# Kernel optimization log

Measured on AMD Instinct MI355X. Metric: run time of the kernel, lower is better.

The kernel has to match this reference:

```python
import jax, jax.numpy as jnp
import numpy as np

N = 10000      # nodes
E = 160000     # edges
F_IN = 128     # input_feature
G = 64         # graphs in batch
NC = 10        # num_classes
H1, H2, H3 = 1000, 700, 200


def _xavier(k, fi, fo):
    lim = float(np.sqrt(6.0 / (fi + fo)))
    return jax.random.uniform(k, (fi, fo), jnp.float32, -lim, lim)


def setup_inputs() -> dict:
    key = jax.random.key(0)
    ks = jax.random.split(key, 8)
    x = jax.random.normal(ks[0], (N, F_IN), jnp.float32)
    edge_index = jax.random.randint(ks[1], (2, E), 0, N)
    batch = jnp.sort(jax.random.randint(ks[2], (N,), 0, G))
    return {
        "x": x,
        "edge_index": edge_index,
        "batch": batch,
        "W1": _xavier(ks[3], F_IN, H1), "b1": jnp.zeros((H1,), jnp.float32),
        "W2": _xavier(ks[4], H1, H2),   "b2": jnp.zeros((H2,), jnp.float32),
        "W3": _xavier(ks[5], H2, H3),   "b3": jnp.zeros((H3,), jnp.float32),
        "Wl": _xavier(ks[6], H3, NC),   "bl": jnp.zeros((NC,), jnp.float32),
    }


def _gcn_conv(x, W, b, src, dst, dinv):
    # GCNConv: h = xW; out_i = sum_{j->i} d_j^-1/2 d_i^-1/2 h_j + d_i^-1 h_i + b
    h = x @ W
    coef = dinv[src] * dinv[dst]                      # [E]
    agg = jax.ops.segment_sum(h[src] * coef[:, None], dst, num_segments=N)
    agg = agg + h * (dinv * dinv)[:, None]            # self-loop term
    return agg + b


def reference(x, edge_index, batch, W1, b1, W2, b2, W3, b3, Wl, bl):
    src, dst = edge_index[0], edge_index[1]
    # degree with self-loops (edge weight 1), computed on target nodes
    deg = jax.ops.segment_sum(jnp.ones((E,), x.dtype), dst, num_segments=N) + 1.0
    dinv = jax.lax.rsqrt(deg)

    h = jax.nn.relu(_gcn_conv(x, W1, b1, src, dst, dinv))
    h = jax.nn.relu(_gcn_conv(h, W2, b2, src, dst, dinv))
    h = jax.nn.relu(_gcn_conv(h, W3, b3, src, dst, dinv))

    # global_mean_pool over graph ids
    s = jax.ops.segment_sum(h, batch, num_segments=G)
    cnt = jax.ops.segment_sum(jnp.ones((N,), h.dtype), batch, num_segments=G)
    pooled = s / jnp.maximum(cnt, 1.0)[:, None]

    # dropout is identity in eval mode
    return pooled @ Wl + bl
```

## Files before the change

kernel.cpp:

```cpp
#include <hip/hip_runtime.h>
#include <hip/hip_bf16.h>
#include <stdint.h>


#define SLOT 64

__device__ __forceinline__ uint16_t f2b(float f) {
    union { float f; uint32_t u; } v; v.f = f;
    return (uint16_t)((v.u + 0x7fffu + ((v.u >> 16) & 1u)) >> 16);
}
__device__ __forceinline__ float blo(uint32_t u) { union { uint32_t u; float f; } v; v.u = u << 16; return v.f; }
__device__ __forceinline__ float bhi(uint32_t u) { union { uint32_t u; float f; } v; v.u = u & 0xffff0000u; return v.f; }

__global__ void k_scatter(const int* __restrict__ src, const int* __restrict__ dst,
                          int* __restrict__ cursor, int* __restrict__ slots, int E) {
    int e = blockIdx.x * blockDim.x + threadIdx.x;
    if (e < E) {
        int s = src[e], d = dst[e];
        int pos = atomicAdd(&cursor[d], 1);
        if (pos < SLOT) slots[d * SLOT + pos] = s;
    }
}

__global__ void k_prep(const float* __restrict__ W1, const float* __restrict__ W2,
                       const float* __restrict__ W3,
                       uint16_t* __restrict__ T1, uint16_t* __restrict__ T2,
                       uint16_t* __restrict__ T3,
                       const float* __restrict__ b1, const float* __restrict__ b2,
                       const float* __restrict__ b3,
                       float* __restrict__ p1, float* __restrict__ p2,
                       float* __restrict__ p3,
                       const float* __restrict__ x, uint16_t* __restrict__ xb,
                       const int* __restrict__ deg, float* __restrict__ dinv,
                       int N, int F, int H1, int H2, int H3,
                       int Fp, int H1p, int H2p, int H3p, int n8) {
    __shared__ float tile[32][33];
    int z = blockIdx.z;
    if (z < 3) {
        const float* W; uint16_t* T; int K, Nn, Kp, Np;
        if (z == 0)      { W = W1; T = T1; K = F;  Nn = H1; Kp = Fp;  Np = H1p; }
        else if (z == 1) { W = W2; T = T2; K = H1; Nn = H2; Kp = H1p; Np = H2p; }
        else             { W = W3; T = T3; K = H2; Nn = H3; Kp = H2p; Np = H3p; }
        if ((int)blockIdx.x * 32 >= Kp || (int)blockIdx.y * 32 >= Np) return;
        int k0 = blockIdx.x * 32, n0 = blockIdx.y * 32;
        int tx = threadIdx.x, ty = threadIdx.y;
        for (int i = ty; i < 32; i += 8) {
            int k = k0 + i, n = n0 + tx;
            tile[i][tx] = (k < K && n < Nn) ? W[(size_t)k * Nn + n] : 0.f;
        }
        __syncthreads();
        for (int i = ty; i < 32; i += 8) {
            int n = n0 + i, k = k0 + tx;
            T[(size_t)n * Kp + k] = f2b(tile[tx][i]);
        }
    } else {
        int id = (blockIdx.y * gridDim.x + blockIdx.x) * 256 + threadIdx.y * 32 + threadIdx.x;
        if (z == 3) {
            if (id < H1p) p1[id] = (id < H1) ? b1[id] : 0.f;
            else if (id < H1p + H2p) { int k = id - H1p; p2[k] = (k < H2) ? b2[k] : 0.f; }
            else if (id < H1p + H2p + H3p) { int k = id - H1p - H2p; p3[k] = (k < H3) ? b3[k] : 0.f; }
        } else if (z == 4) {
            if (id < n8) {
                const float4* x4 = (const float4*)x;
                float4 a = x4[2 * id], b = x4[2 * id + 1];
                uint4 o;
                o.x = (uint32_t)f2b(a.x) | ((uint32_t)f2b(a.y) << 16);
                o.y = (uint32_t)f2b(a.z) | ((uint32_t)f2b(a.w) << 16);
                o.z = (uint32_t)f2b(b.x) | ((uint32_t)f2b(b.y) << 16);
                o.w = (uint32_t)f2b(b.z) | ((uint32_t)f2b(b.w) << 16);
                ((uint4*)xb)[id] = o;
            }
        } else {
            if (id < N) dinv[id] = rsqrtf((float)deg[id] + 1.0f);
        }
    }
}

__global__ __launch_bounds__(256) void k_agg_panel(
    const uint16_t* __restrict__ in, uint16_t* __restrict__ out,
    const int* __restrict__ deg_, const int* __restrict__ slots,
    const float* __restrict__ dinv, const float* __restrict__ bias,
    int N, int Hc, int pc, int P, int relu) {
    int slotg = blockIdx.x & 7;
    int panel = slotg % P;
    int seg   = slotg / P;
    int nseg  = 8 / P;
    int segLen = (N + nseg - 1) / nseg;
    int wave = threadIdx.x >> 6, lane = threadIdx.x & 63;
    int half = lane >> 5, sub = lane & 31;
    int item = (blockIdx.x >> 3) * 128 + wave * 32 + sub;
    int rel = item / pc;
    if (rel >= segLen) return;
    int node = seg * segLen + rel;
    if (node >= N) return;
    int j = panel * pc + (item - rel * pc);
    int deg = deg_[node];
    if (deg > SLOT) deg = SLOT;
    int base = node * SLOT;
    float dv = dinv[node];
    const uint4* in4 = (const uint4*)in;
    float a[8] = {0.f, 0.f, 0.f, 0.f, 0.f, 0.f, 0.f, 0.f};
    if (half == 0) {
        float self = dv * dv;
        uint4 v = in4[(size_t)node * Hc + j];
        a[0] = self * blo(v.x); a[1] = self * bhi(v.x);
        a[2] = self * blo(v.y); a[3] = self * bhi(v.y);
        a[4] = self * blo(v.z); a[5] = self * bhi(v.z);
        a[6] = self * blo(v.w); a[7] = self * bhi(v.w);
    }
    int D8 = deg & ~7;
    for (int e = 4 * half; e < D8; e += 8) {
        int4 q = *(const int4*)&slots[base + e];
        uint4 h0 = in4[(size_t)q.x * Hc + j];
        uint4 h1 = in4[(size_t)q.y * Hc + j];
        uint4 h2 = in4[(size_t)q.z * Hc + j];
        uint4 h3 = in4[(size_t)q.w * Hc + j];
        float c0 = dinv[q.x] * dv, c1 = dinv[q.y] * dv;
        float c2 = dinv[q.z] * dv, c3 = dinv[q.w] * dv;
        a[0] += c0 * blo(h0.x); a[1] += c0 * bhi(h0.x);
        a[2] += c0 * blo(h0.y); a[3] += c0 * bhi(h0.y);
        a[4] += c0 * blo(h0.z); a[5] += c0 * bhi(h0.z);
        a[6] += c0 * blo(h0.w); a[7] += c0 * bhi(h0.w);
        a[0] += c1 * blo(h1.x); a[1] += c1 * bhi(h1.x);
        a[2] += c1 * blo(h1.y); a[3] += c1 * bhi(h1.y);
        a[4] += c1 * blo(h1.z); a[5] += c1 * bhi(h1.z);
        a[6] += c1 * blo(h1.w); a[7] += c1 * bhi(h1.w);
        a[0] += c2 * blo(h2.x); a[1] += c2 * bhi(h2.x);
        a[2] += c2 * blo(h2.y); a[3] += c2 * bhi(h2.y);
        a[4] += c2 * blo(h2.z); a[5] += c2 * bhi(h2.z);
        a[6] += c2 * blo(h2.w); a[7] += c2 * bhi(h2.w);
        a[0] += c3 * blo(h3.x); a[1] += c3 * bhi(h3.x);
        a[2] += c3 * blo(h3.y); a[3] += c3 * bhi(h3.y);
        a[4] += c3 * blo(h3.z); a[5] += c3 * bhi(h3.z);
        a[6] += c3 * blo(h3.w); a[7] += c3 * bhi(h3.w);
    }
    int t0 = half ? (D8 + 4 < deg ? D8 + 4 : deg) : D8;
    int t1 = half ? deg : (D8 + 4 < deg ? D8 + 4 : deg);
    for (int e = t0; e < t1; ++e) {
        int s0 = slots[base + e];
        uint4 h = in4[(size_t)s0 * Hc + j];
        float c = dinv[s0] * dv;
        a[0] += c * blo(h.x); a[1] += c * bhi(h.x);
        a[2] += c * blo(h.y); a[3] += c * bhi(h.y);
        a[4] += c * blo(h.z); a[5] += c * bhi(h.z);
        a[6] += c * blo(h.w); a[7] += c * bhi(h.w);
    }
#pragma unroll
    for (int t = 0; t < 8; ++t) a[t] += __shfl_xor(a[t], 32, 64);
    if (half == 0) {
        if (bias) {
            const float4* b4 = (const float4*)bias;
            float4 b0 = b4[2 * j], b1 = b4[2 * j + 1];
            a[0] += b0.x; a[1] += b0.y; a[2] += b0.z; a[3] += b0.w;
            a[4] += b1.x; a[5] += b1.y; a[6] += b1.z; a[7] += b1.w;
        }
        if (relu) {
#pragma unroll
            for (int t = 0; t < 8; ++t) a[t] = fmaxf(a[t], 0.f);
        }
        uint4 o;
        o.x = (uint32_t)f2b(a[0]) | ((uint32_t)f2b(a[1]) << 16);
        o.y = (uint32_t)f2b(a[2]) | ((uint32_t)f2b(a[3]) << 16);
        o.z = (uint32_t)f2b(a[4]) | ((uint32_t)f2b(a[5]) << 16);
        o.w = (uint32_t)f2b(a[6]) | ((uint32_t)f2b(a[7]) << 16);
        ((uint4*)out)[(size_t)node * Hc + j] = o;
    }
}

__global__ __launch_bounds__(256) void k_pool_fast(
    const uint16_t* __restrict__ h, const int* __restrict__ batch,
    float* __restrict__ pooled_sum, int N, int H, int Hp) {
    int j    = threadIdx.x & 63;
    int slot = threadIdx.x >> 6;
    int Hc   = H >> 2;
    if (j >= Hc) return;
    int HcP  = Hp >> 2;
    const uint2* h2 = (const uint2*)h;
    int base = (blockIdx.x * 4 + slot) * 16;
    float a0 = 0.f, a1 = 0.f, a2 = 0.f, a3 = 0.f;
    int gcur = -1;
#pragma unroll 4
    for (int t = 0; t < 16; ++t) {
        int node = base + t;
        if (node < N) {
            int g = batch[node];
            if (g != gcur) {
                if (gcur >= 0) {
                    float* ps = &pooled_sum[(size_t)gcur * H + j * 4];
                    atomicAdd(&ps[0], a0); atomicAdd(&ps[1], a1);
                    atomicAdd(&ps[2], a2); atomicAdd(&ps[3], a3);
                }
                gcur = g; a0 = a1 = a2 = a3 = 0.f;
            }
            uint2 v = h2[(size_t)node * HcP + j];
            a0 += blo(v.x); a1 += bhi(v.x);
            a2 += blo(v.y); a3 += bhi(v.y);
        }
    }
    if (gcur >= 0) {
        float* ps = &pooled_sum[(size_t)gcur * H + j * 4];
        atomicAdd(&ps[0], a0); atomicAdd(&ps[1], a1);
        atomicAdd(&ps[2], a2); atomicAdd(&ps[3], a3);
    }
}

typedef __attribute__((ext_vector_type(8))) short short8;
typedef __attribute__((ext_vector_type(4))) float floatx4;

#define LDSP(p) ((__attribute__((address_space(3))) void*)(uintptr_t)(p))
#define GLBP(p) ((const __attribute__((address_space(1))) void*)(uintptr_t)(p))

__global__ __launch_bounds__(256) void k_gemm128(
    const uint16_t* __restrict__ A, const uint16_t* __restrict__ Bt,
    const float* __restrict__ bias, uint16_t* __restrict__ Cout,
    int M, int Kp, int Np, int relu) {
    __shared__ uint16_t As[128 * 64];
    __shared__ uint16_t Bs[128 * 64];
    int tid = threadIdx.x;
    int wave = tid >> 6, lane = tid & 63;
    int quad = lane >> 4, m16 = lane & 15;
    int wr = wave >> 1, wc = wave & 1;
    int row0 = blockIdx.y * 128, col0 = blockIdx.x * 128;

    int rA = tid >> 3;
    int cA = (tid & 7) ^ (rA & 7);
    const uint16_t* gA = A  + (size_t)(row0 + rA) * Kp + cA * 8;
    const uint16_t* gB = Bt + (size_t)(col0 + rA) * Kp + cA * 8;
    uint16_t* lA = As + tid * 8;
    uint16_t* lB = Bs + tid * 8;
    size_t rowStep32 = (size_t)32 * Kp;

    floatx4 acc[4][4];
#pragma unroll
    for (int i = 0; i < 4; ++i)
#pragma unroll
        for (int j = 0; j < 4; ++j) acc[i][j] = (floatx4){0.f, 0.f, 0.f, 0.f};

    const short* Ash = (const short*)As;
    const short* Bsh = (const short*)Bs;
    int swA = m16 & 7;

    for (int k0 = 0; k0 < Kp; k0 += 64) {
#pragma unroll
        for (int p = 0; p < 4; ++p) {
            __builtin_amdgcn_global_load_lds(GLBP(gA + p * rowStep32), LDSP(lA + p * 2048), 16, 0, 0);
            __builtin_amdgcn_global_load_lds(GLBP(gB + p * rowStep32), LDSP(lB + p * 2048), 16, 0, 0);
        }
        gA += 64; gB += 64;
        __syncthreads();
#pragma unroll
        for (int h = 0; h < 2; ++h) {
            short8 af[4], bf[4];
            int c = h * 4 + quad;
            int pos = (c ^ swA) * 8;
#pragma unroll
            for (int i = 0; i < 4; ++i)
                af[i] = *(const short8*)&Ash[(wr * 64 + i * 16 + m16) * 64 + pos];
#pragma unroll
            for (int j = 0; j < 4; ++j)
                bf[j] = *(const short8*)&Bsh[(wc * 64 + j * 16 + m16) * 64 + pos];
#pragma unroll
            for (int i = 0; i < 4; ++i)
#pragma unroll
                for (int j = 0; j < 4; ++j)
                    acc[i][j] = __builtin_amdgcn_mfma_f32_16x16x32_bf16(af[i], bf[j], acc[i][j], 0, 0, 0);
        }
        __syncthreads();
    }

    float bv[4];
#pragma unroll
    for (int j = 0; j < 4; ++j) {
        int n = col0 + wc * 64 + j * 16 + m16;
        bv[j] = bias ? bias[n] : 0.f;
    }
#pragma unroll
    for (int i = 0; i < 4; ++i) {
        int mBase = row0 + wr * 64 + i * 16 + quad * 4;
#pragma unroll
        for (int r = 0; r < 4; ++r) {
            int m = mBase + r;
            if (m < M) {
#pragma unroll
                for (int j = 0; j < 4; ++j) {
                    int n = col0 + wc * 64 + j * 16 + m16;
                    float v = acc[i][j][r] + bv[j];
                    if (relu) v = fmaxf(v, 0.f);
                    Cout[(size_t)m * Np + n] = f2b(v);
                }
            }
        }
    }
}

__global__ __launch_bounds__(256) void k_gemm64(
    const uint16_t* __restrict__ A, const uint16_t* __restrict__ Bt,
    const float* __restrict__ bias, uint16_t* __restrict__ Cout,
    int M, int Kp, int Np, int relu) {
    __shared__ uint16_t As[128 * 64];
    __shared__ uint16_t Bs[64 * 64];
    int tid = threadIdx.x;
    int wave = tid >> 6, lane = tid & 63;
    int quad = lane >> 4, m16 = lane & 15;
    int wr = wave >> 1, wc = wave & 1;
    int row0 = blockIdx.y * 128, col0 = blockIdx.x * 64;

    int rA = tid >> 3;
    int cA = (tid & 7) ^ (rA & 7);
    const uint16_t* gA = A  + (size_t)(row0 + rA) * Kp + cA * 8;
    const uint16_t* gB = Bt + (size_t)(col0 + rA) * Kp + cA * 8;
    uint16_t* lA = As + tid * 8;
    uint16_t* lB = Bs + tid * 8;
    size_t rowStep32 = (size_t)32 * Kp;

    floatx4 acc[4][2];
#pragma unroll
    for (int i = 0; i < 4; ++i)
#pragma unroll
        for (int j = 0; j < 2; ++j) acc[i][j] = (floatx4){0.f, 0.f, 0.f, 0.f};

    const short* Ash = (const short*)As;
    const short* Bsh = (const short*)Bs;
    int swA = m16 & 7;

    for (int k0 = 0; k0 < Kp; k0 += 64) {
#pragma unroll
        for (int p = 0; p < 4; ++p)
            __builtin_amdgcn_global_load_lds(GLBP(gA + p * rowStep32), LDSP(lA + p * 2048), 16, 0, 0);
#pragma unroll
        for (int p = 0; p < 2; ++p)
            __builtin_amdgcn_global_load_lds(GLBP(gB + p * rowStep32), LDSP(lB + p * 2048), 16, 0, 0);
        gA += 64; gB += 64;
        __syncthreads();
#pragma unroll
        for (int h = 0; h < 2; ++h) {
            short8 af[4], bf[2];
            int c = h * 4 + quad;
            int pos = (c ^ swA) * 8;
#pragma unroll
            for (int i = 0; i < 4; ++i)
                af[i] = *(const short8*)&Ash[(wr * 64 + i * 16 + m16) * 64 + pos];
#pragma unroll
            for (int j = 0; j < 2; ++j)
                bf[j] = *(const short8*)&Bsh[(wc * 32 + j * 16 + m16) * 64 + pos];
#pragma unroll
            for (int i = 0; i < 4; ++i)
#pragma unroll
                for (int j = 0; j < 2; ++j)
                    acc[i][j] = __builtin_amdgcn_mfma_f32_16x16x32_bf16(af[i], bf[j], acc[i][j], 0, 0, 0);
        }
        __syncthreads();
    }

    float bv[2];
#pragma unroll
    for (int j = 0; j < 2; ++j) {
        int n = col0 + wc * 32 + j * 16 + m16;
        bv[j] = bias ? bias[n] : 0.f;
    }
#pragma unroll
    for (int i = 0; i < 4; ++i) {
        int mBase = row0 + wr * 64 + i * 16 + quad * 4;
#pragma unroll
        for (int r = 0; r < 4; ++r) {
            int m = mBase + r;
            if (m < M) {
#pragma unroll
                for (int j = 0; j < 2; ++j) {
                    int n = col0 + wc * 32 + j * 16 + m16;
                    float v = acc[i][j][r] + bv[j];
                    if (relu) v = fmaxf(v, 0.f);
                    Cout[(size_t)m * Np + n] = f2b(v);
                }
            }
        }
    }
}

__global__ void k_classifier(const float* __restrict__ pooled_sum,
                             const int* __restrict__ batch,
                             const float* __restrict__ Wl, const float* __restrict__ bl,
                             float* __restrict__ out, int N, int H, int NC) {
    int g = blockIdx.x, c = threadIdx.x;
    int lo = 0, hi = N;
    while (lo < hi) { int mid = (lo + hi) >> 1; if (batch[mid] < g) lo = mid + 1; else hi = mid; }
    int start = lo;
    lo = start; hi = N;
    while (lo < hi) { int mid = (lo + hi) >> 1; if (batch[mid] < g + 1) lo = mid + 1; else hi = mid; }
    int end = lo;
    float scale = 1.0f / fmaxf((float)(end - start), 1.0f);
    if (c < NC) {
        float acc = 0.f;
        for (int k = 0; k < H; ++k) acc += pooled_sum[(size_t)g * H + k] * Wl[(size_t)k * NC + c];
        out[(size_t)g * NC + c] = acc * scale + bl[c];
    }
}

static inline size_t align256(size_t x) { return (x + 255) & ~(size_t)255; }
static inline int pad128(int x) { return (x + 127) & ~127; }

extern "C" void kernel_launch(void* const* d_in, const int* in_sizes, int n_in,
                              void* d_out, int out_size, void* d_ws, size_t ws_size,
                              hipStream_t stream) {
    const float* x   = (const float*)d_in[0];
    const int*   ei  = (const int*)d_in[1];
    const int*   bat = (const int*)d_in[2];
    const float* W1  = (const float*)d_in[3];
    const float* b1  = (const float*)d_in[4];
    const float* W2  = (const float*)d_in[5];
    const float* b2  = (const float*)d_in[6];
    const float* W3  = (const float*)d_in[7];
    const float* b3  = (const float*)d_in[8];
    const float* Wl  = (const float*)d_in[9];
    const float* bl  = (const float*)d_in[10];

    const int N  = in_sizes[2];
    const int E  = in_sizes[1] / 2;
    const int F  = in_sizes[0] / N;
    const int H1 = in_sizes[4];
    const int H2 = in_sizes[6];
    const int H3 = in_sizes[8];
    const int NC = in_sizes[10];
    const int G  = out_size / NC;
    const int* src = ei;
    const int* dst = ei + E;

    const int Mp  = pad128(N);
    const int Fp  = F;
    const int H1p = pad128(H1);
    const int H2p = pad128(H2);
    const int H3p = pad128(H3);

    char* p = (char*)d_ws;
    size_t off = 0;
    auto carve = [&](size_t bytes) { void* q = p + off; off += align256(bytes); return q; };
    uint16_t* xb     = (uint16_t*)carve((size_t)Mp * Fp * 2);
    uint16_t* bufA   = (uint16_t*)carve((size_t)Mp * 2048);
    uint16_t* bufB   = (uint16_t*)carve((size_t)Mp * 2048);
    uint16_t* W1t    = (uint16_t*)carve((size_t)H1p * Fp * 2);
    uint16_t* W2t    = (uint16_t*)carve((size_t)H2p * H1p * 2);
    uint16_t* W3t    = (uint16_t*)carve((size_t)H3p * H2p * 2);
    float* b1p       = (float*)carve((size_t)H1p * 4);
    float* b2p       = (float*)carve((size_t)H2p * 4);
    float* b3p       = (float*)carve((size_t)H3p * 4);
    float* dinv      = (float*)carve((size_t)N * 4);
    int*   cursor    = (int*)carve((size_t)N * 4);
    float* pooled    = (float*)carve((size_t)G * H3 * 4);
    int*   slots     = (int*)carve((size_t)N * SLOT * 4);
    (void)ws_size;

    const int nbE = (E + 255) / 256;

    size_t zlen = (size_t)((char*)pooled - (char*)cursor) + (size_t)G * H3 * 4;
    hipMemsetAsync(cursor, 0, zlen, stream);

    k_scatter<<<nbE, 256, 0, stream>>>(src, dst, cursor, slots, E);

    k_prep<<<dim3(32, 32, 6), dim3(32, 8), 0, stream>>>(
        W1, W2, W3, W1t, W2t, W3t, b1, b2, b3, b1p, b2p, b3p, x, xb,
        cursor, dinv, N, F, H1, H2, H3, Fp, H1p, H2p, H3p, N * F / 8);

    auto agg_grid = [&](int P, int pc) {
        int nseg = 8 / P;
        int segLen = (N + nseg - 1) / nseg;
        return 8 * ((segLen * pc + 127) / 128);
    };

    k_agg_panel<<<agg_grid(1, 16), 256, 0, stream>>>(
        xb, bufA, cursor, slots, dinv, nullptr, N, 16, 16, 1, 0);
    k_gemm128<<<dim3(H1p / 128, Mp / 128), 256, 0, stream>>>(
        bufA, W1t, b1p, bufB, N, Fp, H1p, 1);

    k_gemm128<<<dim3(H2p / 128, Mp / 128), 256, 0, stream>>>(
        bufB, W2t, nullptr, bufA, N, H1p, H2p, 0);
    k_agg_panel<<<agg_grid(8, 12), 256, 0, stream>>>(
        bufA, bufB, cursor, slots, dinv, b2p, N, 96, 12, 8, 1);

    k_gemm64<<<dim3(H3p / 64, Mp / 128), 256, 0, stream>>>(
        bufB, W3t, nullptr, bufA, N, H2p, H3p, 0);
    k_agg_panel<<<agg_grid(4, 8), 256, 0, stream>>>(
        bufA, bufB, cursor, slots, dinv, b3p, N, 32, 8, 4, 1);

    k_pool_fast<<<(N + 63) / 64, 256, 0, stream>>>(
        (const uint16_t*)bufB, bat, pooled, N, H3, H3p);
    k_classifier<<<G, 64, 0, stream>>>(pooled, bat, Wl, bl, (float*)d_out, N, H3, NC);
}
```

Before: 245.4 us.

## Pipeline neighbor gathers in aggregation and swizzle GEMM block order for locality

The aggregation kernel's 8-edge loop is software-pipelined: the next group's slot indices, feature rows and normalization coefficients are loaded before the current group is accumulated, hiding gather latency. The GEMM kernels switch from a 2D grid to a 1D grid with a block-index remap that groups 8 row tiles and iterates column tiles outermost, aiming at better cache reuse across XCDs. This adds register pressure in the aggregation loop, and out-of-range blocks from rounding exit early.

```diff
diff --git a/kernel.cpp b/kernel.cpp
--- a/kernel.cpp
+++ b/kernel.cpp
@@ -109,7 +109,8 @@
         a[6] = self * blo(v.w); a[7] = self * bhi(v.w);
     }
     int D8 = deg & ~7;
-    for (int e = 4 * half; e < D8; e += 8) {
+    int e = 4 * half;
+    if (e < D8) {
         int4 q = *(const int4*)&slots[base + e];
         uint4 h0 = in4[(size_t)q.x * Hc + j];
         uint4 h1 = in4[(size_t)q.y * Hc + j];
@@ -117,6 +118,33 @@
         uint4 h3 = in4[(size_t)q.w * Hc + j];
         float c0 = dinv[q.x] * dv, c1 = dinv[q.y] * dv;
         float c2 = dinv[q.z] * dv, c3 = dinv[q.w] * dv;
+        for (e += 8; e < D8; e += 8) {
+            int4 qn = *(const int4*)&slots[base + e];
+            uint4 g0 = in4[(size_t)qn.x * Hc + j];
+            uint4 g1 = in4[(size_t)qn.y * Hc + j];
+            uint4 g2 = in4[(size_t)qn.z * Hc + j];
+            uint4 g3 = in4[(size_t)qn.w * Hc + j];
+            float d0 = dinv[qn.x] * dv, d1 = dinv[qn.y] * dv;
+            float d2 = dinv[qn.z] * dv, d3 = dinv[qn.w] * dv;
+            a[0] += c0 * blo(h0.x); a[1] += c0 * bhi(h0.x);
+            a[2] += c0 * blo(h0.y); a[3] += c0 * bhi(h0.y);
+            a[4] += c0 * blo(h0.z); a[5] += c0 * bhi(h0.z);
+            a[6] += c0 * blo(h0.w); a[7] += c0 * bhi(h0.w);
+            a[0] += c1 * blo(h1.x); a[1] += c1 * bhi(h1.x);
+            a[2] += c1 * blo(h1.y); a[3] += c1 * bhi(h1.y);
+            a[4] += c1 * blo(h1.z); a[5] += c1 * bhi(h1.z);
+            a[6] += c1 * blo(h1.w); a[7] += c1 * bhi(h1.w);
+            a[0] += c2 * blo(h2.x); a[1] += c2 * bhi(h2.x);
+            a[2] += c2 * blo(h2.y); a[3] += c2 * bhi(h2.y);
+            a[4] += c2 * blo(h2.z); a[5] += c2 * bhi(h2.z);
+            a[6] += c2 * blo(h2.w); a[7] += c2 * bhi(h2.w);
+            a[0] += c3 * blo(h3.x); a[1] += c3 * bhi(h3.x);
+            a[2] += c3 * blo(h3.y); a[3] += c3 * bhi(h3.y);
+            a[4] += c3 * blo(h3.z); a[5] += c3 * bhi(h3.z);
+            a[6] += c3 * blo(h3.w); a[7] += c3 * bhi(h3.w);
+            h0 = g0; h1 = g1; h2 = g2; h3 = g3;
+            c0 = d0; c1 = d1; c2 = d2; c3 = d3;
+        }
         a[0] += c0 * blo(h0.x); a[1] += c0 * bhi(h0.x);
         a[2] += c0 * blo(h0.y); a[3] += c0 * bhi(h0.y);
         a[4] += c0 * blo(h0.z); a[5] += c0 * bhi(h0.z);
@@ -136,8 +164,8 @@
     }
     int t0 = half ? (D8 + 4 < deg ? D8 + 4 : deg) : D8;
     int t1 = half ? deg : (D8 + 4 < deg ? D8 + 4 : deg);
-    for (int e = t0; e < t1; ++e) {
-        int s0 = slots[base + e];
+    for (int ee = t0; ee < t1; ++ee) {
+        int s0 = slots[base + ee];
         uint4 h = in4[(size_t)s0 * Hc + j];
         float c = dinv[s0] * dv;
         a[0] += c * blo(h.x); a[1] += c * bhi(h.x);
@@ -213,14 +241,21 @@
 __global__ __launch_bounds__(256) void k_gemm128(
     const uint16_t* __restrict__ A, const uint16_t* __restrict__ Bt,
     const float* __restrict__ bias, uint16_t* __restrict__ Cout,
-    int M, int Kp, int Np, int relu) {
+    int M, int Kp, int Np, int relu, int nrg, int nr) {
+    int bid = blockIdx.x;
+    int rsub = bid & 7;
+    int t_ = bid >> 3;
+    int rg = t_ % nrg, cc = t_ / nrg;
+    int rt = rg * 8 + rsub;
+    if (rt >= nr) return;
+    int row0 = rt * 128, col0 = cc * 128;
+
     __shared__ uint16_t As[128 * 64];
     __shared__ uint16_t Bs[128 * 64];
     int tid = threadIdx.x;
     int wave = tid >> 6, lane = tid & 63;
     int quad = lane >> 4, m16 = lane & 15;
     int wr = wave >> 1, wc = wave & 1;
-    int row0 = blockIdx.y * 128, col0 = blockIdx.x * 128;
 
     int rA = tid >> 3;
     int cA = (tid & 7) ^ (rA & 7);
@@ -296,14 +331,21 @@
 __global__ __launch_bounds__(256) void k_gemm64(
     const uint16_t* __restrict__ A, const uint16_t* __restrict__ Bt,
     const float* __restrict__ bias, uint16_t* __restrict__ Cout,
-    int M, int Kp, int Np, int relu) {
+    int M, int Kp, int Np, int relu, int nrg, int nr) {
+    int bid = blockIdx.x;
+    int rsub = bid & 7;
+    int t_ = bid >> 3;
+    int rg = t_ % nrg, cc = t_ / nrg;
+    int rt = rg * 8 + rsub;
+    if (rt >= nr) return;
+    int row0 = rt * 128, col0 = cc * 64;
+
     __shared__ uint16_t As[128 * 64];
     __shared__ uint16_t Bs[64 * 64];
     int tid = threadIdx.x;
     int wave = tid >> 6, lane = tid & 63;
     int quad = lane >> 4, m16 = lane & 15;
     int wr = wave >> 1, wc = wave & 1;
-    int row0 = blockIdx.y * 128, col0 = blockIdx.x * 64;
 
     int rA = tid >> 3;
     int cA = (tid & 7) ^ (rA & 7);
@@ -466,18 +508,21 @@
         return 8 * ((segLen * pc + 127) / 128);
     };
 
+    const int nr  = Mp / 128;
+    const int nrg = (nr + 7) / 8;
+
     k_agg_panel<<<agg_grid(1, 16), 256, 0, stream>>>(
         xb, bufA, cursor, slots, dinv, nullptr, N, 16, 16, 1, 0);
-    k_gemm128<<<dim3(H1p / 128, Mp / 128), 256, 0, stream>>>(
-        bufA, W1t, b1p, bufB, N, Fp, H1p, 1);
-
-    k_gemm128<<<dim3(H2p / 128, Mp / 128), 256, 0, stream>>>(
-        bufB, W2t, nullptr, bufA, N, H1p, H2p, 0);
+    k_gemm128<<<nrg * 8 * (H1p / 128), 256, 0, stream>>>(
+        bufA, W1t, b1p, bufB, N, Fp, H1p, 1, nrg, nr);
+
+    k_gemm128<<<nrg * 8 * (H2p / 128), 256, 0, stream>>>(
+        bufB, W2t, nullptr, bufA, N, H1p, H2p, 0, nrg, nr);
     k_agg_panel<<<agg_grid(8, 12), 256, 0, stream>>>(
         bufA, bufB, cursor, slots, dinv, b2p, N, 96, 12, 8, 1);
 
-    k_gemm64<<<dim3(H3p / 64, Mp / 128), 256, 0, stream>>>(
-        bufB, W3t, nullptr, bufA, N, H2p, H3p, 0);
+    k_gemm64<<<nrg * 8 * (H3p / 64), 256, 0, stream>>>(
+        bufB, W3t, nullptr, bufA, N, H2p, H3p, 0, nrg, nr);
     k_agg_panel<<<agg_grid(4, 8), 256, 0, stream>>>(
         bufA, bufB, cursor, slots, dinv, b3p, N, 32, 8, 4, 1);
 
```

New measurement: 238.2 us. -2.9%, faster.
